# Kernel optimization log

Measured on AMD Instinct MI355X. Metric: run time of the kernel, lower is better.

## Reference

```python
import math
import jax, jax.numpy as jnp
import numpy as np

NUM_HEADS = 16

def setup_inputs() -> dict:
    key = jax.random.key(0)
    k1, k2, k3, k4, k5 = jax.random.split(key, 5)
    B, S, D = 8, 4096, 1024
    x = jax.random.normal(k1, (B, S, D), dtype=jnp.float32)
    W_qkv = jax.random.normal(k2, (D, 3 * D), dtype=jnp.float32) * (1.0 / math.sqrt(D))
    b_qkv = jax.random.normal(k3, (3 * D,), dtype=jnp.float32) * 0.02
    W_out = jax.random.normal(k4, (D, D), dtype=jnp.float32) * (1.0 / math.sqrt(D))
    b_out = jax.random.normal(k5, (D,), dtype=jnp.float32) * 0.02
    return {"x": x, "W_qkv": W_qkv, "b_qkv": b_qkv, "W_out": W_out, "b_out": b_out}

def reference(x, W_qkv, b_qkv, W_out, b_out):
    B, S, D = x.shape
    H = NUM_HEADS
    hd = D // H
    scale = 1.0 / math.sqrt(hd)
    # QKV projection: (B,S,D) -> (B,S,3D), reshaped to (B,S,H,3*hd)
    qkv = (x @ W_qkv + b_qkv).reshape(B, S, H, 3 * hd)
    q, k, v = jnp.split(qkv, 3, axis=-1)  # each (B,S,H,hd)
    # Faithful to source: no head permute, so attention is across the H heads
    # at each (batch, seq) position. scores: (B,S,H,H)
    scores = jnp.einsum('bsqd,bskd->bsqk', q, k) * scale
    attn = jax.nn.softmax(scores, axis=-1)
    values = jnp.einsum('bsqk,bskd->bsqd', attn, v).reshape(B, S, D)
    return values @ W_out + b_out
```

## Files before the change

### kernel.cpp

```cpp
#include <hip/hip_runtime.h>
#include <hip/hip_bf16.h>

#define TOKENS   32768
#define DMODEL   1024
#define THREE_D  3072

using u16 = unsigned short;
typedef __attribute__((ext_vector_type(8))) short short8;
typedef __attribute__((ext_vector_type(4))) float f32x4;

__device__ __forceinline__ float bf2f(u16 u) {
  union { unsigned int i; float f; } v; v.i = ((unsigned int)u) << 16; return v.f;
}
__device__ __forceinline__ u16 f2bf(float f) {
  __hip_bfloat16 h = __float2bfloat16(f);
  return *reinterpret_cast<u16*>(&h);
}

__device__ __forceinline__ void gload_lds16(const u16* g, u16* l) {
  __builtin_amdgcn_global_load_lds((const __attribute__((address_space(1))) void*)g,
                                   (__attribute__((address_space(3))) void*)l,
                                   16, 0, 0);
}

__global__ __launch_bounds__(256) void convert_f32_bf16(const float* __restrict__ in,
                                                        u16* __restrict__ out, long n) {
  long i = ((long)blockIdx.x * 256 + threadIdx.x) * 4;
  if (i >= n) return;
  float4 v = *reinterpret_cast<const float4*>(in + i);
  ushort4 o;
  o.x = f2bf(v.x); o.y = f2bf(v.y); o.z = f2bf(v.z); o.w = f2bf(v.w);
  *reinterpret_cast<ushort4*>(out + i) = o;
}

__global__ __launch_bounds__(256) void transpose_convert(const float* __restrict__ in,
                                                         u16* __restrict__ out,
                                                         int R, int C) {
  __shared__ u16 tile[32][33];
  const int bc = blockIdx.x * 32;
  const int br = blockIdx.y * 32;
  const int tx = threadIdx.x & 31;
  const int ty = threadIdx.x >> 5;
  #pragma unroll
  for (int i = 0; i < 32; i += 8)
    tile[ty + i][tx] = f2bf(in[(long)(br + ty + i) * C + bc + tx]);
  __syncthreads();
  #pragma unroll
  for (int i = 0; i < 32; i += 8)
    out[(long)(bc + ty + i) * R + br + tx] = tile[tx][ty + i];
}

#define BM 256
#define BN 256
#define BK 64

#define VM4 asm volatile("s_waitcnt vmcnt(4)" ::: "memory")
#define VM0 asm volatile("s_waitcnt vmcnt(0)" ::: "memory")
#define VMN ((void)0)
#define NOSTAGE ((void)0)

#define STAGE_A(T, H)                                                          \
  { _Pragma("unroll") for (int j_ = 0; j_ < 2; j_++) {                         \
      const int lr_ = (H) * 128 + (wave * 2 + j_) * 8;                         \
      gload_lds16(A + (long)(bm + lr_ + sr) * a_stride + (long)(T) * a_grp + scol, \
                  &As[(T) & 1][lr_ * BK]);                                     \
  } }
#define STAGE_B(T, H)                                                          \
  { _Pragma("unroll") for (int j_ = 0; j_ < 2; j_++) {                         \
      const int lr_ = (H) * 128 + (wave * 2 + j_) * 8;                         \
      gload_lds16(BT + (long)(bn + lr_ + sr) * K + (T) * BK + scol,            \
                  &Bs[(T) & 1][lr_ * BK]);                                     \
  } }

#define PHASE(BUF, QR, QC, RDA, STAGE, VMW)                                    \
  {                                                                            \
    if (RDA) {                                                                 \
      _Pragma("unroll") for (int mi = 0; mi < 2; mi++)                         \
        _Pragma("unroll") for (int kh = 0; kh < 2; kh++)                       \
          a[mi][kh] = *reinterpret_cast<const short8*>(                        \
              &As[BUF][((QR) * 128 + wrow + mi * 16 + lrow) * BK +             \
                       (((kh * 4 + quad) ^ xs) * 8)]);                         \
    }                                                                          \
    short8 b[4][2];                                                            \
    _Pragma("unroll") for (int ni = 0; ni < 4; ni++)                           \
      _Pragma("unroll") for (int kh = 0; kh < 2; kh++)                         \
        b[ni][kh] = *reinterpret_cast<const short8*>(                          \
            &Bs[BUF][((QC) * 128 + wcol + ni * 16 + lrow) * BK +               \
                     (((kh * 4 + quad) ^ xs) * 8)]);                           \
    STAGE;                                                                     \
    VMW;                                                                       \
    __builtin_amdgcn_s_barrier();                                              \
    asm volatile("s_waitcnt lgkmcnt(0)" ::: "memory");                         \
    __builtin_amdgcn_sched_barrier(0);                                         \
    __builtin_amdgcn_s_setprio(1);                                             \
    _Pragma("unroll") for (int mi = 0; mi < 2; mi++)                           \
      _Pragma("unroll") for (int ni = 0; ni < 4; ni++) {                       \
        acc[QR][QC][mi][ni] = __builtin_amdgcn_mfma_f32_16x16x32_bf16(         \
            a[mi][0], b[ni][0], acc[QR][QC][mi][ni], 0, 0, 0);                 \
        acc[QR][QC][mi][ni] = __builtin_amdgcn_mfma_f32_16x16x32_bf16(         \
            a[mi][1], b[ni][1], acc[QR][QC][mi][ni], 0, 0, 0);                 \
      }                                                                        \
    __builtin_amdgcn_s_setprio(0);                                             \
    __builtin_amdgcn_s_barrier();                                              \
    __builtin_amdgcn_sched_barrier(0);                                         \
  }

template <bool OUT_F32>
__global__ __launch_bounds__(512, 2) void gemm_bt_bias(
    const u16* __restrict__ A, const u16* __restrict__ BT,
    const float* __restrict__ bias, void* __restrict__ Cv,
    int M, int N, int K, long a_stride, int a_grp) {
  __shared__ alignas(16) u16 As[2][BM * BK];
  __shared__ alignas(16) u16 Bs[2][BN * BK];
  (void)M;

  const int cpx = gridDim.x >> 3;
  const int wg  = ((int)blockIdx.x & 7) * cpx + ((int)blockIdx.x >> 3);
  const int tiles_n = N / BN;
  const int bm = (wg / tiles_n) * BM;
  const int bn = (wg % tiles_n) * BN;

  const int tid  = threadIdx.x;
  const int wave = tid >> 6;
  const int lane = tid & 63;
  const int wrow = (wave & 3) * 32;
  const int wcol = (wave >> 2) * 64;
  const int lrow = lane & 15;
  const int quad = lane >> 4;
  const int xs   = lrow & 7;

  const int sr     = lane >> 3;
  const int schunk = (lane & 7) ^ sr;
  const int scol   = schunk * 8;

  const int NT = K / BK;

  f32x4 acc[2][2][2][4];
  #pragma unroll
  for (int i = 0; i < 2; i++)
    #pragma unroll
    for (int j = 0; j < 2; j++)
      #pragma unroll
      for (int m = 0; m < 2; m++)
        #pragma unroll
        for (int n = 0; n < 4; n++) acc[i][j][m][n] = (f32x4){0.f, 0.f, 0.f, 0.f};

  STAGE_A(0, 0); STAGE_A(0, 1); STAGE_B(0, 0); STAGE_B(0, 1);
  STAGE_A(1, 0); STAGE_B(1, 1);
  VM4;
  __builtin_amdgcn_s_barrier();

  short8 a[2][2];
  #pragma unroll 1
  for (int t = 0; t + 2 < NT; t += 2) {
    PHASE(0, 0, 0, 1, STAGE_A(t + 1, 1), VMN);
    PHASE(0, 0, 1, 0, STAGE_B(t + 1, 0), VMN);
    PHASE(0, 1, 1, 1, STAGE_A(t + 2, 0), VMN);
    PHASE(0, 1, 0, 0, STAGE_B(t + 2, 1), VM4);
    PHASE(1, 0, 0, 1, STAGE_A(t + 2, 1), VMN);
    PHASE(1, 0, 1, 0, STAGE_B(t + 2, 0), VMN);
    PHASE(1, 1, 1, 1, STAGE_A(t + 3, 0), VMN);
    PHASE(1, 1, 0, 0, STAGE_B(t + 3, 1), VM4);
  }
  PHASE(0, 0, 0, 1, STAGE_A(NT - 1, 1), VMN);
  PHASE(0, 0, 1, 0, STAGE_B(NT - 1, 0), VMN);
  PHASE(0, 1, 1, 1, NOSTAGE, VMN);
  PHASE(0, 1, 0, 0, NOSTAGE, VM0);
  PHASE(1, 0, 0, 1, NOSTAGE, VMN);
  PHASE(1, 0, 1, 0, NOSTAGE, VMN);
  PHASE(1, 1, 1, 1, NOSTAGE, VMN);
  PHASE(1, 1, 0, 0, NOSTAGE, VMN);

  #pragma unroll
  for (int qc = 0; qc < 2; qc++) {
    #pragma unroll
    for (int ni = 0; ni < 4; ni++) {
      const int col = bn + qc * 128 + wcol + ni * 16 + lrow;
      const float bv = bias[col];
      #pragma unroll
      for (int qr = 0; qr < 2; qr++) {
        #pragma unroll
        for (int mi = 0; mi < 2; mi++) {
          #pragma unroll
          for (int r = 0; r < 4; r++) {
            const int row = bm + qr * 128 + wrow + mi * 16 + quad * 4 + r;
            const float val = acc[qr][qc][mi][ni][r] + bv;
            if (OUT_F32)
              ((float*)Cv)[(long)row * N + col] = val;
            else
              ((u16*)Cv)[(long)row * N + col] = f2bf(val);
          }
        }
      }
    }
  }
}

__global__ __launch_bounds__(256) void attn_local(u16* __restrict__ qkv) {
  __shared__ float p_s[4][16][16];
  const int tid  = threadIdx.x;
  const int wave = tid >> 6;
  const int lane = tid & 63;
  const int t    = blockIdx.x * 4 + wave;
  u16* row = qkv + (long)t * THREE_D;
  const int lrow = lane & 15;
  const int quad = lane >> 4;
  const int kq   = quad * 8;

  short8 a0 = *reinterpret_cast<const short8*>(row + lrow * 192 + kq);
  short8 a1 = *reinterpret_cast<const short8*>(row + lrow * 192 + 32 + kq);
  short8 b0 = *reinterpret_cast<const short8*>(row + lrow * 192 + 64 + kq);
  short8 b1 = *reinterpret_cast<const short8*>(row + lrow * 192 + 96 + kq);
  f32x4 s = {0.f, 0.f, 0.f, 0.f};
  s = __builtin_amdgcn_mfma_f32_16x16x32_bf16(a0, b0, s, 0, 0, 0);
  s = __builtin_amdgcn_mfma_f32_16x16x32_bf16(a1, b1, s, 0, 0, 0);

  const float scale = 0.125f;
  float p[4];
  #pragma unroll
  for (int r = 0; r < 4; r++) {
    float x = s[r] * scale;
    float m = x;
    #pragma unroll
    for (int mask = 1; mask < 16; mask <<= 1) m = fmaxf(m, __shfl_xor(m, mask));
    float e = __expf(x - m);
    float l = e;
    #pragma unroll
    for (int mask = 1; mask < 16; mask <<= 1) l += __shfl_xor(l, mask);
    p[r] = e / l;
  }
  #pragma unroll
  for (int r = 0; r < 4; r++) p_s[wave][quad * 4 + r][lrow] = p[r];
  __syncthreads();

  float o[16];
  #pragma unroll
  for (int i = 0; i < 16; i++) o[i] = 0.f;
  #pragma unroll
  for (int j = 0; j < 16; j++) {
    float vj = bf2f(row[j * 192 + 128 + lane]);
    #pragma unroll
    for (int i = 0; i < 16; i++) o[i] += p_s[wave][i][j] * vj;
  }
  #pragma unroll
  for (int i = 0; i < 16; i++)
    row[i * 192 + lane] = f2bf(o[i]);
}

extern "C" void kernel_launch(void* const* d_in, const int* in_sizes, int n_in,
                              void* d_out, int out_size, void* d_ws, size_t ws_size,
                              hipStream_t stream) {
  const float* x     = (const float*)d_in[0];
  const float* W_qkv = (const float*)d_in[1];
  const float* b_qkv = (const float*)d_in[2];
  const float* W_out = (const float*)d_in[3];
  const float* b_out = (const float*)d_in[4];
  float* out = (float*)d_out;

  char* ws = (char*)d_ws;
  u16* qkv   = (u16*)ws;  ws += (size_t)TOKENS * THREE_D * 2;
  u16* x_bf  = (u16*)ws;  ws += (size_t)TOKENS * DMODEL * 2;
  u16* wqkvT = (u16*)ws;  ws += (size_t)THREE_D * DMODEL * 2;
  u16* woutT = (u16*)ws;

  dim3 tb(256);
  dim3 gtb(512);
  convert_f32_bf16<<<dim3((TOKENS * DMODEL) / 1024), tb, 0, stream>>>(
      x, x_bf, (long)TOKENS * DMODEL);
  transpose_convert<<<dim3(THREE_D / 32, DMODEL / 32), tb, 0, stream>>>(W_qkv, wqkvT, DMODEL, THREE_D);
  transpose_convert<<<dim3(DMODEL / 32, DMODEL / 32), tb, 0, stream>>>(W_out, woutT, DMODEL, DMODEL);
  gemm_bt_bias<false><<<dim3((TOKENS / BM) * (THREE_D / BN)), gtb, 0, stream>>>(
      x_bf, wqkvT, b_qkv, qkv, TOKENS, THREE_D, DMODEL, (long)DMODEL, 64);
  attn_local<<<dim3(TOKENS / 4), tb, 0, stream>>>(qkv);
  gemm_bt_bias<true><<<dim3((TOKENS / BM) * (DMODEL / BN)), gtb, 0, stream>>>(
      qkv, woutT, b_out, out, TOKENS, DMODEL, DMODEL, (long)THREE_D, 192);
}
```

Measured before the change: 612.0 us.

## Reorder GEMM quadrant phases to reuse B fragments and deepen prefetch

Changes the per-tile quadrant traversal to a serpentine order (00,10,11,01) so that A and B register fragments are each reloaded from LDS only every other phase, which cuts LDS read traffic. The staging schedule is rearranged so more global-to-LDS loads stay in flight, with a vmcnt(6) wait instead of vmcnt(4). The main loop bound and the prologue and epilogue staging change to match. The risk is subtle correctness problems from the new stage/wait ordering and higher register pressure from b living across phases.

```diff
diff --git a/kernel.cpp b/kernel.cpp
--- a/kernel.cpp
+++ b/kernel.cpp
@@ -54,7 +54,7 @@
 #define BN 256
 #define BK 64
 
-#define VM4 asm volatile("s_waitcnt vmcnt(4)" ::: "memory")
+#define VM6 asm volatile("s_waitcnt vmcnt(6)" ::: "memory")
 #define VM0 asm volatile("s_waitcnt vmcnt(0)" ::: "memory")
 #define VMN ((void)0)
 #define NOSTAGE ((void)0)
@@ -72,7 +72,7 @@
                   &Bs[(T) & 1][lr_ * BK]);                                     \
   } }
 
-#define PHASE(BUF, QR, QC, RDA, STAGE, VMW)                                    \
+#define PHASE(BUF, QR, QC, RDA, RDB, STAGE, VMW)                               \
   {                                                                            \
     if (RDA) {                                                                 \
       _Pragma("unroll") for (int mi = 0; mi < 2; mi++)                         \
@@ -81,12 +81,13 @@
               &As[BUF][((QR) * 128 + wrow + mi * 16 + lrow) * BK +             \
                        (((kh * 4 + quad) ^ xs) * 8)]);                         \
     }                                                                          \
-    short8 b[4][2];                                                            \
-    _Pragma("unroll") for (int ni = 0; ni < 4; ni++)                           \
-      _Pragma("unroll") for (int kh = 0; kh < 2; kh++)                         \
-        b[ni][kh] = *reinterpret_cast<const short8*>(                          \
-            &Bs[BUF][((QC) * 128 + wcol + ni * 16 + lrow) * BK +               \
-                     (((kh * 4 + quad) ^ xs) * 8)]);                           \
+    if (RDB) {                                                                 \
+      _Pragma("unroll") for (int ni = 0; ni < 4; ni++)                         \
+        _Pragma("unroll") for (int kh = 0; kh < 2; kh++)                       \
+          b[ni][kh] = *reinterpret_cast<const short8*>(                        \
+              &Bs[BUF][((QC) * 128 + wcol + ni * 16 + lrow) * BK +             \
+                       (((kh * 4 + quad) ^ xs) * 8)]);                         \
+    }                                                                          \
     STAGE;                                                                     \
     VMW;                                                                       \
     __builtin_amdgcn_s_barrier();                                              \
@@ -145,31 +146,32 @@
         #pragma unroll
         for (int n = 0; n < 4; n++) acc[i][j][m][n] = (f32x4){0.f, 0.f, 0.f, 0.f};
 
-  STAGE_A(0, 0); STAGE_A(0, 1); STAGE_B(0, 0); STAGE_B(0, 1);
-  STAGE_A(1, 0); STAGE_B(1, 1);
-  VM4;
+  STAGE_A(0, 0); STAGE_B(0, 0); STAGE_A(0, 1); STAGE_B(0, 1);
+  STAGE_B(1, 0); STAGE_A(1, 1); STAGE_B(1, 1);
+  VM6;
   __builtin_amdgcn_s_barrier();
 
   short8 a[2][2];
+  short8 b[4][2];
   #pragma unroll 1
-  for (int t = 0; t + 2 < NT; t += 2) {
-    PHASE(0, 0, 0, 1, STAGE_A(t + 1, 1), VMN);
-    PHASE(0, 0, 1, 0, STAGE_B(t + 1, 0), VMN);
-    PHASE(0, 1, 1, 1, STAGE_A(t + 2, 0), VMN);
-    PHASE(0, 1, 0, 0, STAGE_B(t + 2, 1), VM4);
-    PHASE(1, 0, 0, 1, STAGE_A(t + 2, 1), VMN);
-    PHASE(1, 0, 1, 0, STAGE_B(t + 2, 0), VMN);
-    PHASE(1, 1, 1, 1, STAGE_A(t + 3, 0), VMN);
-    PHASE(1, 1, 0, 0, STAGE_B(t + 3, 1), VM4);
-  }
-  PHASE(0, 0, 0, 1, STAGE_A(NT - 1, 1), VMN);
-  PHASE(0, 0, 1, 0, STAGE_B(NT - 1, 0), VMN);
-  PHASE(0, 1, 1, 1, NOSTAGE, VMN);
-  PHASE(0, 1, 0, 0, NOSTAGE, VM0);
-  PHASE(1, 0, 0, 1, NOSTAGE, VMN);
-  PHASE(1, 0, 1, 0, NOSTAGE, VMN);
-  PHASE(1, 1, 1, 1, NOSTAGE, VMN);
-  PHASE(1, 1, 0, 0, NOSTAGE, VMN);
+  for (int t = 0; t + 3 < NT; t += 2) {
+    PHASE(0, 0, 0, 1, 1, STAGE_A(t + 1, 0), VMN);
+    PHASE(0, 1, 0, 1, 0, STAGE_B(t + 2, 0), VMN);
+    PHASE(0, 1, 1, 0, 1, STAGE_A(t + 2, 1), VMN);
+    PHASE(0, 0, 1, 1, 0, STAGE_B(t + 2, 1), VM6);
+    PHASE(1, 0, 0, 1, 1, STAGE_A(t + 2, 0), VMN);
+    PHASE(1, 1, 0, 1, 0, STAGE_B(t + 3, 0), VMN);
+    PHASE(1, 1, 1, 0, 1, STAGE_A(t + 3, 1), VMN);
+    PHASE(1, 0, 1, 1, 0, STAGE_B(t + 3, 1), VM6);
+  }
+  PHASE(0, 0, 0, 1, 1, STAGE_A(NT - 1, 0), VMN);
+  PHASE(0, 1, 0, 1, 0, NOSTAGE, VMN);
+  PHASE(0, 1, 1, 0, 1, NOSTAGE, VMN);
+  PHASE(0, 0, 1, 1, 0, NOSTAGE, VM0);
+  PHASE(1, 0, 0, 1, 1, NOSTAGE, VMN);
+  PHASE(1, 1, 0, 1, 0, NOSTAGE, VMN);
+  PHASE(1, 1, 1, 0, 1, NOSTAGE, VMN);
+  PHASE(1, 0, 1, 1, 0, NOSTAGE, VMN);
 
   #pragma unroll
   for (int qc = 0; qc < 2; qc++) {
```

Result: faster. 599.6 us (-2.0%).

## Switch GEMM to 32x32x16 MFMA with register double-buffered LDS reads

Applied to the files above, without the earlier changes.

Replaces the 16x16x32 MFMA quadrant-phase GEMM with 32x32x16 MFMAs over a 128x64 per-wave tile. LDS fragment reads are double-buffered in registers and overlapped with MMAs through partial lgkmcnt waits. The global-to-LDS staging schedule is reworked to load a whole K tile per half-loop and wait with vmcnt(0). The goal is fewer LDS reads per FLOP and better MFMA issue density. The cost is more register pressure, and the full vmcnt drains may expose global load latency.

```diff
diff --git a/kernel.cpp b/kernel.cpp
--- a/kernel.cpp
+++ b/kernel.cpp
@@ -8,6 +8,7 @@
 using u16 = unsigned short;
 typedef __attribute__((ext_vector_type(8))) short short8;
 typedef __attribute__((ext_vector_type(4))) float f32x4;
+typedef __attribute__((ext_vector_type(16))) float f32x16;
 
 __device__ __forceinline__ float bf2f(u16 u) {
   union { unsigned int i; float f; } v; v.i = ((unsigned int)u) << 16; return v.f;
@@ -54,10 +55,13 @@
 #define BN 256
 #define BK 64
 
-#define VM4 asm volatile("s_waitcnt vmcnt(4)" ::: "memory")
-#define VM0 asm volatile("s_waitcnt vmcnt(0)" ::: "memory")
-#define VMN ((void)0)
-#define NOSTAGE ((void)0)
+#define LGKM6 { asm volatile("s_waitcnt lgkmcnt(6)" ::: "memory"); \
+                __builtin_amdgcn_sched_barrier(0); }
+#define LGKM0 { asm volatile("s_waitcnt lgkmcnt(0)" ::: "memory"); \
+                __builtin_amdgcn_sched_barrier(0); }
+#define VMW0  asm volatile("s_waitcnt vmcnt(0)" ::: "memory")
+#define BARR  { __builtin_amdgcn_sched_barrier(0); __builtin_amdgcn_s_barrier(); \
+                __builtin_amdgcn_sched_barrier(0); }
 
 #define STAGE_A(T, H)                                                          \
   { _Pragma("unroll") for (int j_ = 0; j_ < 2; j_++) {                         \
@@ -72,38 +76,21 @@
                   &Bs[(T) & 1][lr_ * BK]);                                     \
   } }
 
-#define PHASE(BUF, QR, QC, RDA, STAGE, VMW)                                    \
-  {                                                                            \
-    if (RDA) {                                                                 \
-      _Pragma("unroll") for (int mi = 0; mi < 2; mi++)                         \
-        _Pragma("unroll") for (int kh = 0; kh < 2; kh++)                       \
-          a[mi][kh] = *reinterpret_cast<const short8*>(                        \
-              &As[BUF][((QR) * 128 + wrow + mi * 16 + lrow) * BK +             \
-                       (((kh * 4 + quad) ^ xs) * 8)]);                         \
-    }                                                                          \
-    short8 b[4][2];                                                            \
-    _Pragma("unroll") for (int ni = 0; ni < 4; ni++)                           \
-      _Pragma("unroll") for (int kh = 0; kh < 2; kh++)                         \
-        b[ni][kh] = *reinterpret_cast<const short8*>(                          \
-            &Bs[BUF][((QC) * 128 + wcol + ni * 16 + lrow) * BK +               \
-                     (((kh * 4 + quad) ^ xs) * 8)]);                           \
-    STAGE;                                                                     \
-    VMW;                                                                       \
-    __builtin_amdgcn_s_barrier();                                              \
-    asm volatile("s_waitcnt lgkmcnt(0)" ::: "memory");                         \
-    __builtin_amdgcn_sched_barrier(0);                                         \
-    __builtin_amdgcn_s_setprio(1);                                             \
-    _Pragma("unroll") for (int mi = 0; mi < 2; mi++)                           \
-      _Pragma("unroll") for (int ni = 0; ni < 4; ni++) {                       \
-        acc[QR][QC][mi][ni] = __builtin_amdgcn_mfma_f32_16x16x32_bf16(         \
-            a[mi][0], b[ni][0], acc[QR][QC][mi][ni], 0, 0, 0);                 \
-        acc[QR][QC][mi][ni] = __builtin_amdgcn_mfma_f32_16x16x32_bf16(         \
-            a[mi][1], b[ni][1], acc[QR][QC][mi][ni], 0, 0, 0);                 \
-      }                                                                        \
-    __builtin_amdgcn_s_setprio(0);                                             \
-    __builtin_amdgcn_s_barrier();                                              \
-    __builtin_amdgcn_sched_barrier(0);                                         \
-  }
+#define READS(SET, BUF, KS)                                                    \
+  { _Pragma("unroll") for (int f_ = 0; f_ < 4; f_++)                           \
+      a[SET][f_] = *reinterpret_cast<const short8*>(                           \
+          &As[BUF][(wm + f_ * 32 + l31) * BK + ((((KS) * 2 + kh) ^ xr) * 8)]); \
+    _Pragma("unroll") for (int g_ = 0; g_ < 2; g_++)                           \
+      b[SET][g_] = *reinterpret_cast<const short8*>(                           \
+          &Bs[BUF][(wn + g_ * 32 + l31) * BK + ((((KS) * 2 + kh) ^ xr) * 8)]); }
+
+#define MMA(SET)                                                               \
+  { __builtin_amdgcn_s_setprio(1);                                             \
+    _Pragma("unroll") for (int mf_ = 0; mf_ < 4; mf_++)                        \
+      _Pragma("unroll") for (int nf_ = 0; nf_ < 2; nf_++)                      \
+        acc[mf_][nf_] = __builtin_amdgcn_mfma_f32_32x32x16_bf16(               \
+            a[SET][mf_], b[SET][nf_], acc[mf_][nf_], 0, 0, 0);                 \
+    __builtin_amdgcn_s_setprio(0); }
 
 template <bool OUT_F32>
 __global__ __launch_bounds__(512, 2) void gemm_bt_bias(
@@ -123,11 +110,11 @@
   const int tid  = threadIdx.x;
   const int wave = tid >> 6;
   const int lane = tid & 63;
-  const int wrow = (wave & 3) * 32;
-  const int wcol = (wave >> 2) * 64;
-  const int lrow = lane & 15;
-  const int quad = lane >> 4;
-  const int xs   = lrow & 7;
+  const int wm   = (wave >> 2) * 128;
+  const int wn   = (wave & 3) * 64;
+  const int l31  = lane & 31;
+  const int kh   = lane >> 5;
+  const int xr   = l31 & 7;
 
   const int sr     = lane >> 3;
   const int schunk = (lane & 7) ^ sr;
@@ -135,62 +122,56 @@
 
   const int NT = K / BK;
 
-  f32x4 acc[2][2][2][4];
-  #pragma unroll
-  for (int i = 0; i < 2; i++)
+  f32x16 acc[4][2];
+  #pragma unroll
+  for (int i = 0; i < 4; i++)
     #pragma unroll
     for (int j = 0; j < 2; j++)
       #pragma unroll
-      for (int m = 0; m < 2; m++)
-        #pragma unroll
-        for (int n = 0; n < 4; n++) acc[i][j][m][n] = (f32x4){0.f, 0.f, 0.f, 0.f};
+      for (int r = 0; r < 16; r++) acc[i][j][r] = 0.f;
 
   STAGE_A(0, 0); STAGE_A(0, 1); STAGE_B(0, 0); STAGE_B(0, 1);
-  STAGE_A(1, 0); STAGE_B(1, 1);
-  VM4;
+  VMW0;
   __builtin_amdgcn_s_barrier();
 
-  short8 a[2][2];
+  short8 a[2][4];
+  short8 b[2][2];
+  READS(0, 0, 0);
+
   #pragma unroll 1
   for (int t = 0; t + 2 < NT; t += 2) {
-    PHASE(0, 0, 0, 1, STAGE_A(t + 1, 1), VMN);
-    PHASE(0, 0, 1, 0, STAGE_B(t + 1, 0), VMN);
-    PHASE(0, 1, 1, 1, STAGE_A(t + 2, 0), VMN);
-    PHASE(0, 1, 0, 0, STAGE_B(t + 2, 1), VM4);
-    PHASE(1, 0, 0, 1, STAGE_A(t + 2, 1), VMN);
-    PHASE(1, 0, 1, 0, STAGE_B(t + 2, 0), VMN);
-    PHASE(1, 1, 1, 1, STAGE_A(t + 3, 0), VMN);
-    PHASE(1, 1, 0, 0, STAGE_B(t + 3, 1), VM4);
-  }
-  PHASE(0, 0, 0, 1, STAGE_A(NT - 1, 1), VMN);
-  PHASE(0, 0, 1, 0, STAGE_B(NT - 1, 0), VMN);
-  PHASE(0, 1, 1, 1, NOSTAGE, VMN);
-  PHASE(0, 1, 0, 0, NOSTAGE, VM0);
-  PHASE(1, 0, 0, 1, NOSTAGE, VMN);
-  PHASE(1, 0, 1, 0, NOSTAGE, VMN);
-  PHASE(1, 1, 1, 1, NOSTAGE, VMN);
-  PHASE(1, 1, 0, 0, NOSTAGE, VMN);
-
-  #pragma unroll
-  for (int qc = 0; qc < 2; qc++) {
-    #pragma unroll
-    for (int ni = 0; ni < 4; ni++) {
-      const int col = bn + qc * 128 + wcol + ni * 16 + lrow;
-      const float bv = bias[col];
+    BARR; READS(1, 0, 1); STAGE_A(t + 1, 0); STAGE_A(t + 1, 1); LGKM6; MMA(0);
+    BARR; READS(0, 0, 2); STAGE_B(t + 1, 0); STAGE_B(t + 1, 1); LGKM6; MMA(1);
+    BARR; READS(1, 0, 3);                                       LGKM6; MMA(0); VMW0;
+    BARR; READS(0, 1, 0);                                       LGKM6; MMA(1);
+    BARR; READS(1, 1, 1); STAGE_A(t + 2, 0); STAGE_A(t + 2, 1); LGKM6; MMA(0);
+    BARR; READS(0, 1, 2); STAGE_B(t + 2, 0); STAGE_B(t + 2, 1); LGKM6; MMA(1);
+    BARR; READS(1, 1, 3);                                       LGKM6; MMA(0); VMW0;
+    BARR; READS(0, 0, 0);                                       LGKM6; MMA(1);
+  }
+  BARR; READS(1, 0, 1); STAGE_A(NT - 1, 0); STAGE_A(NT - 1, 1); LGKM6; MMA(0);
+  BARR; READS(0, 0, 2); STAGE_B(NT - 1, 0); STAGE_B(NT - 1, 1); LGKM6; MMA(1);
+  BARR; READS(1, 0, 3);                                         LGKM6; MMA(0); VMW0;
+  BARR; READS(0, 1, 0);                                         LGKM6; MMA(1);
+  BARR; READS(1, 1, 1);                                         LGKM6; MMA(0);
+  BARR; READS(0, 1, 2);                                         LGKM6; MMA(1);
+  BARR; READS(1, 1, 3);                                         LGKM6; MMA(0);
+  BARR;                                                         LGKM0; MMA(1);
+
+  #pragma unroll
+  for (int nf = 0; nf < 2; nf++) {
+    const int col = bn + wn + nf * 32 + l31;
+    const float bv = bias[col];
+    #pragma unroll
+    for (int mf = 0; mf < 4; mf++) {
       #pragma unroll
-      for (int qr = 0; qr < 2; qr++) {
-        #pragma unroll
-        for (int mi = 0; mi < 2; mi++) {
-          #pragma unroll
-          for (int r = 0; r < 4; r++) {
-            const int row = bm + qr * 128 + wrow + mi * 16 + quad * 4 + r;
-            const float val = acc[qr][qc][mi][ni][r] + bv;
-            if (OUT_F32)
-              ((float*)Cv)[(long)row * N + col] = val;
-            else
-              ((u16*)Cv)[(long)row * N + col] = f2bf(val);
-          }
-        }
+      for (int r = 0; r < 16; r++) {
+        const int row = bm + wm + mf * 32 + (r & 3) + 8 * (r >> 2) + 4 * kh;
+        const float val = acc[mf][nf][r] + bv;
+        if (OUT_F32)
+          ((float*)Cv)[(long)row * N + col] = val;
+        else
+          ((u16*)Cv)[(long)row * N + col] = f2bf(val);
       }
     }
   }
```

Result: faster. 580.1 us (-5.2%).
